# Kernel optimization log

Hardware: AMD Instinct MI355X
Metric: run time of the kernel (lower is better)

## Reference

```python
import jax, jax.numpy as jnp
import numpy as np

E = 128  # embedding dim (edim)
NEG_INF = -1e8


def setup_inputs() -> dict:
    key = jax.random.key(0)
    ks = jax.random.split(key, 12)
    n_users, n_items, B, L = 100000, 50000, 4096, 64
    s = 1.0 / np.sqrt(2 * E)
    return {
        "user_embs": jax.random.normal(ks[0], (n_users, E), jnp.float32),
        "item_embs": jax.random.normal(ks[1], (n_items, E), jnp.float32),
        "w_uu": jax.random.normal(ks[2], (2 * E,), jnp.float32) * s,
        "w_uiu": jax.random.normal(ks[3], (2 * E,), jnp.float32) * s,
        "w_uui": jax.random.normal(ks[4], (2 * E,), jnp.float32) * s,
        "W0": jax.random.normal(ks[5], (E, E // 2), jnp.float32) / np.sqrt(E),
        "b0": jax.random.normal(ks[6], (E // 2,), jnp.float32) * 0.01,
        "w1": jax.random.normal(ks[7], (E // 2,), jnp.float32) / np.sqrt(E // 2),
        "uid": jax.random.randint(ks[8], (B,), 0, n_users),
        "nbr": jax.random.randint(ks[9], (B, L), 0, n_users),
        "uiu": jax.random.randint(ks[10], (B, 2, L), 0, n_items),
        "uui": jax.random.randint(ks[11], (B, 2, L), 0, n_items),
    }


def reference(user_embs, item_embs, w_uu, w_uiu, w_uui, W0, b0, w1, uid, nbr, uiu, uui):
    self_emb = user_embs[uid][:, None, :]  # [B,1,E]

    def branch(feat, mask, w):
        # feat: [B,L,E], mask: [B,L] bool. concat([self,feat]) @ w split into two GEMVs.
        logits = self_emb @ w[:E, None] + feat @ w[E:, None]  # [B,L,1]
        logits = jax.nn.leaky_relu(logits)  # slope 0.01, matches F.leaky_relu default
        logits = logits + NEG_INF * mask[:, :, None].astype(feat.dtype)
        a = jax.nn.softmax(logits, axis=1)  # over neighbor dim
        return jax.nn.relu(jnp.sum(a * feat, axis=1))  # [B,E]

    # uu meta-path
    uu_feat = branch((self_emb + user_embs[nbr]) * 0.5, nbr == 0, w_uu)
    # uiu meta-path: row 0 = item ids, row 1 = user ids
    mp_iid, mp_uid = uiu[:, 0], uiu[:, 1]
    uiu_feat = branch((self_emb + item_embs[mp_iid] + user_embs[mp_uid]) / 3.0, mp_iid == 0, w_uiu)
    # uui meta-path: row 0 = user ids, row 1 = item ids
    mp_uid2, mp_iid2 = uui[:, 0], uui[:, 1]
    uui_feat = branch((self_emb + user_embs[mp_uid2] + item_embs[mp_iid2]) / 3.0, mp_uid2 == 0, w_uui)

    def inter(feat):
        return jnp.tanh(feat @ W0 + b0).mean(axis=0) @ w1  # scalar

    scores = jnp.stack([inter(uu_feat), inter(uiu_feat), inter(uui_feat)])
    mp = jax.nn.softmax(scores)
    return jax.nn.relu(mp[0] * uu_feat + mp[1] * uiu_feat + mp[2] * uui_feat)
```

## Files before the change

### kernel.cpp

```cpp
#include <hip/hip_runtime.h>

#define E_DIM 128
#define L_DIM 64
#define HDIM 64

__device__ __forceinline__ float waveSum(float v) {
#pragma unroll
  for (int o = 32; o > 0; o >>= 1) v += __shfl_xor(v, o);
  return v;
}
__device__ __forceinline__ float waveMax(float v) {
#pragma unroll
  for (int o = 32; o > 0; o >>= 1) v = fmaxf(v, __shfl_xor(v, o));
  return v;
}
__device__ __forceinline__ float halfSum(float v) {
#pragma unroll
  for (int o = 16; o > 0; o >>= 1) v += __shfl_xor(v, o);
  return v;
}
__device__ __forceinline__ float halfMax(float v) {
#pragma unroll
  for (int o = 16; o > 0; o >>= 1) v = fmaxf(v, __shfl_xor(v, o));
  return v;
}


__global__ __launch_bounds__(256) void convert_i8(
    const float* __restrict__ user_src, const float* __restrict__ item_src,
    signed char* __restrict__ user_q, signed char* __restrict__ item_q,
    const float* __restrict__ w_uu, const float* __restrict__ w_uiu,
    const float* __restrict__ w_uui, float2* __restrict__ qU0,
    float2* __restrict__ qU1, float2* __restrict__ qU2,
    float2* __restrict__ qI1, float2* __restrict__ qI2, int nUr, int nIr) {
  const int lane = threadIdx.x & 63;
  const int j = lane & 31;
  const int h = lane >> 5;
  const int gw = blockIdx.x * 4 + (threadIdx.x >> 6);
  const int r_all = gw * 2 + h;
  if (r_all >= nUr + nIr) return;

  const bool is_user = (r_all < nUr);
  const int r = is_user ? r_all : r_all - nUr;
  const float* src = is_user ? user_src : item_src;
  signed char* dst = is_user ? user_q : item_q;

  const float4 v = *(const float4*)(src + (long)r * E_DIM + j * 4);

  float am =
      fmaxf(fmaxf(fabsf(v.x), fabsf(v.y)), fmaxf(fabsf(v.z), fabsf(v.w)));
  am = halfMax(am);
  const float s = am * (1.0f / 127.0f);
  const float inv = (am > 0.f) ? 127.0f / am : 0.f;

  int q0 = __float2int_rn(v.x * inv);
  int q1 = __float2int_rn(v.y * inv);
  int q2 = __float2int_rn(v.z * inv);
  int q3 = __float2int_rn(v.w * inv);
  q0 = max(-127, min(127, q0));
  q1 = max(-127, min(127, q1));
  q2 = max(-127, min(127, q2));
  q3 = max(-127, min(127, q3));
  const unsigned int pk = (unsigned int)(q0 & 255) |
                          ((unsigned int)(q1 & 255) << 8) |
                          ((unsigned int)(q2 & 255) << 16) |
                          ((unsigned int)(q3 & 255) << 24);
  ((unsigned int*)dst)[(long)r * (E_DIM / 4) + j] = pk;

  const float* wA = is_user ? w_uu : w_uiu;
  const float* wB = is_user ? w_uiu : w_uui;
  const float4 a4 = *(const float4*)(wA + E_DIM + j * 4);
  const float dA = halfSum(v.x * a4.x + v.y * a4.y + v.z * a4.z + v.w * a4.w);
  const float4 b4 = *(const float4*)(wB + E_DIM + j * 4);
  const float dB = halfSum(v.x * b4.x + v.y * b4.y + v.z * b4.z + v.w * b4.w);
  float dC = 0.f;
  if (is_user) {
    const float4 c4 = *(const float4*)(w_uui + E_DIM + j * 4);
    dC = halfSum(v.x * c4.x + v.y * c4.y + v.z * c4.z + v.w * c4.w);
  }
  if (j == 0) {
    if (is_user) {
      qU0[r] = make_float2(dA, s);
      qU1[r] = make_float2(dB, s);
      qU2[r] = make_float2(dC, s);
    } else {
      qI1[r] = make_float2(dA, s);
      qI2[r] = make_float2(dB, s);
    }
  }
}

__global__ __launch_bounds__(256) void phase1_i8(
    const float* __restrict__ user_embs,
    const signed char* __restrict__ user_q,
    const signed char* __restrict__ item_q,
    const float2* __restrict__ qU0, const float2* __restrict__ qU1,
    const float2* __restrict__ qU2, const float2* __restrict__ qI1,
    const float2* __restrict__ qI2,
    const float* __restrict__ w_uu, const float* __restrict__ w_uiu,
    const float* __restrict__ w_uui, const float* __restrict__ W0,
    const float* __restrict__ b0, const float* __restrict__ w1,
    const int* __restrict__ uid, const int* __restrict__ nbr,
    const int* __restrict__ uiu, const int* __restrict__ uui,
    float* __restrict__ feats,
    float* __restrict__ partials,
    int B) {
  const int lane = threadIdx.x & 63;
  const int j = lane & 15;
  const int quarter = lane >> 4;
  const int wv = threadIdx.x >> 6;
  const int w_id = blockIdx.x * 4 + wv;
  const int b = w_id / 3;
  const int k = w_id - 3 * b;
  if (b >= B) return;

  __shared__ float sc[4][E_DIM];

  const bool is_uu = (k == 0);
  const float scale = is_uu ? 0.5f : (1.0f / 3.0f);
  const uint2* T0 = (const uint2*)((k == 1) ? item_q : user_q);
  const uint2* T1 = (const uint2*)((k == 1) ? user_q : item_q);
  const float2* P0 = (k == 0) ? qU0 : (k == 1) ? qI1 : qU2;
  const float2* P1 = (k == 1) ? qU1 : qI2;

  int i0_l, i1_l;
  if (is_uu) {
    i0_l = nbr[b * L_DIM + lane];
    i1_l = 0;
  } else {
    const int* mp = (k == 1) ? uiu : uui;
    i0_l = mp[(b * 2 + 0) * L_DIM + lane];
    i1_l = mp[(b * 2 + 1) * L_DIM + lane];
  }
  const float2 ps0 = P0[i0_l];
  float2 ps1 = make_float2(0.f, 0.f);
  if (!is_uu) ps1 = P1[i1_l];

  const int u = uid[b];
  const float2 self2 = *(const float2*)(user_embs + (long)u * E_DIM + lane * 2);

  const float* w = (k == 0) ? w_uu : (k == 1) ? w_uiu : w_uui;
  const float2 wa = *(const float2*)(w + lane * 2);
  const float2 wb = *(const float2*)(w + E_DIM + lane * 2);
  const float S1 = waveSum(self2.x * wa.x + self2.y * wa.y);
  const float S2 = waveSum(self2.x * wb.x + self2.y * wb.y);

  float d = ps0.x;
  if (!is_uu) d += ps1.x;
  float logit = S1 + scale * (S2 + d);
  logit = (logit > 0.f) ? logit : 0.01f * logit;
  if (i0_l == 0) logit += -100000000.0f;

  const float M = waveMax(logit);
  const float p = __expf(logit - M);
  const float Z = waveSum(p);
  const float a_l = p / Z;

  const float as0_l = a_l * ps0.y;
  const float as1_l = is_uu ? 0.f : a_l * ps1.y;

  constexpr int RQ = E_DIM / 8;
  float o0 = 0.f, o1 = 0.f, o2 = 0.f, o3 = 0.f;
  float o4 = 0.f, o5 = 0.f, o6 = 0.f, o7 = 0.f;

  int l4 = quarter;
  float a0c = __shfl(as0_l, l4);
  float a1c = 0.f;
  int i0 = __shfl(i0_l, l4);
  uint2 q0 = T0[(long)i0 * RQ + j];
  uint2 q1 = make_uint2(0, 0);
  if (!is_uu) {
    a1c = __shfl(as1_l, l4);
    const int i1 = __shfl(i1_l, l4);
    q1 = T1[(long)i1 * RQ + j];
  }

  for (int it = 0; it < L_DIM / 4; ++it) {
    const float a0 = a0c, a1 = a1c;
    const uint2 qa = q0, qb = q1;
    if (it < L_DIM / 4 - 1) {
      l4 = 4 * (it + 1) + quarter;
      a0c = __shfl(as0_l, l4);
      i0 = __shfl(i0_l, l4);
      q0 = T0[(long)i0 * RQ + j];
      if (!is_uu) {
        a1c = __shfl(as1_l, l4);
        const int i1 = __shfl(i1_l, l4);
        q1 = T1[(long)i1 * RQ + j];
      }
    }
    o0 += a0 * (float)(signed char)(qa.x);
    o1 += a0 * (float)(signed char)(qa.x >> 8);
    o2 += a0 * (float)(signed char)(qa.x >> 16);
    o3 += a0 * (float)((int)qa.x >> 24);
    o4 += a0 * (float)(signed char)(qa.y);
    o5 += a0 * (float)(signed char)(qa.y >> 8);
    o6 += a0 * (float)(signed char)(qa.y >> 16);
    o7 += a0 * (float)((int)qa.y >> 24);
    if (!is_uu) {
      o0 += a1 * (float)(signed char)(qb.x);
      o1 += a1 * (float)(signed char)(qb.x >> 8);
      o2 += a1 * (float)(signed char)(qb.x >> 16);
      o3 += a1 * (float)((int)qb.x >> 24);
      o4 += a1 * (float)(signed char)(qb.y);
      o5 += a1 * (float)(signed char)(qb.y >> 8);
      o6 += a1 * (float)(signed char)(qb.y >> 16);
      o7 += a1 * (float)((int)qb.y >> 24);
    }
  }
  o0 += __shfl_xor(o0, 16); o0 += __shfl_xor(o0, 32);
  o1 += __shfl_xor(o1, 16); o1 += __shfl_xor(o1, 32);
  o2 += __shfl_xor(o2, 16); o2 += __shfl_xor(o2, 32);
  o3 += __shfl_xor(o3, 16); o3 += __shfl_xor(o3, 32);
  o4 += __shfl_xor(o4, 16); o4 += __shfl_xor(o4, 32);
  o5 += __shfl_xor(o5, 16); o5 += __shfl_xor(o5, 32);
  o6 += __shfl_xor(o6, 16); o6 += __shfl_xor(o6, 32);
  o7 += __shfl_xor(o7, 16); o7 += __shfl_xor(o7, 32);

  const float4 sA = *(const float4*)(user_embs + (long)u * E_DIM + j * 8);
  const float4 sB = *(const float4*)(user_embs + (long)u * E_DIM + j * 8 + 4);
  float4 rA, rB;
  rA.x = fmaxf((sA.x + o0) * scale, 0.f);
  rA.y = fmaxf((sA.y + o1) * scale, 0.f);
  rA.z = fmaxf((sA.z + o2) * scale, 0.f);
  rA.w = fmaxf((sA.w + o3) * scale, 0.f);
  rB.x = fmaxf((sB.x + o4) * scale, 0.f);
  rB.y = fmaxf((sB.y + o5) * scale, 0.f);
  rB.z = fmaxf((sB.z + o6) * scale, 0.f);
  rB.w = fmaxf((sB.w + o7) * scale, 0.f);
  if (lane < 16) {
    float* fp = feats + ((long)k * B + b) * E_DIM + j * 8;
    *(float4*)fp = rA;
    *(float4*)(fp + 4) = rB;
    *(float4*)(&sc[wv][j * 8]) = rA;
    *(float4*)(&sc[wv][j * 8 + 4]) = rB;
  }
  __syncthreads();

  float hid = b0[lane];
#pragma unroll 4
  for (int e = 0; e < E_DIM; ++e) hid += sc[wv][e] * W0[e * HDIM + lane];
  const float pp = tanhf(hid) * w1[lane];
  const float sum = waveSum(pp);
  if (lane == 0) partials[(long)k * B + b] = sum;
}

__global__ __launch_bounds__(256) void phase1_f32(
    const float* __restrict__ user_embs, const float* __restrict__ item_embs,
    const float* __restrict__ w_uu, const float* __restrict__ w_uiu,
    const float* __restrict__ w_uui, const float* __restrict__ W0,
    const float* __restrict__ b0, const float* __restrict__ w1,
    const int* __restrict__ uid, const int* __restrict__ nbr,
    const int* __restrict__ uiu, const int* __restrict__ uui,
    float* __restrict__ feats, float* __restrict__ partials, int B) {
  const int lane = threadIdx.x & 63;
  const int wv = threadIdx.x >> 6;
  const int w_id = blockIdx.x * 4 + wv;
  const int b = w_id / 3;
  const int k = w_id - 3 * b;
  if (b >= B) return;

  __shared__ float sc[4][E_DIM];
  const int u = uid[b];
  const float self0 = user_embs[u * E_DIM + lane];
  const float self1 = user_embs[u * E_DIM + 64 + lane];
  const float* w = (k == 0) ? w_uu : (k == 1) ? w_uiu : w_uui;
  const float wa0 = w[lane], wa1 = w[64 + lane];
  const float wb0 = w[128 + lane], wb1 = w[192 + lane];
  const float logit_self = waveSum(self0 * wa0 + self1 * wa1);
  const bool is_uu = (k == 0);
  const float scale = is_uu ? 0.5f : (1.0f / 3.0f);
  const float* t0 = (k == 1) ? item_embs : user_embs;
  const float* t1 = (k == 1) ? user_embs : item_embs;
  int i0_l, i1_l;
  if (is_uu) {
    i0_l = nbr[b * L_DIM + lane];
    i1_l = 0;
  } else {
    const int* mp = (k == 1) ? uiu : uui;
    i0_l = mp[(b * 2 + 0) * L_DIM + lane];
    i1_l = mp[(b * 2 + 1) * L_DIM + lane];
  }
  const float mask_l = (i0_l == 0) ? 1.0f : 0.0f;
  float m = -3.0e38f, s = 0.0f, o0 = 0.0f, o1 = 0.0f;
  int i0 = __shfl(i0_l, 0), i1 = __shfl(i1_l, 0);
  float g00 = t0[i0 * E_DIM + lane];
  float g01 = t0[i0 * E_DIM + 64 + lane];
  float g10 = 0.f, g11 = 0.f;
  if (!is_uu) {
    g10 = t1[i1 * E_DIM + lane];
    g11 = t1[i1 * E_DIM + 64 + lane];
  }
  for (int l = 0; l < L_DIM; ++l) {
    const float f0 = (self0 + g00 + g10) * scale;
    const float f1 = (self1 + g01 + g11) * scale;
    if (l < L_DIM - 1) {
      i0 = __shfl(i0_l, l + 1);
      i1 = __shfl(i1_l, l + 1);
      g00 = t0[i0 * E_DIM + lane];
      g01 = t0[i0 * E_DIM + 64 + lane];
      if (!is_uu) {
        g10 = t1[i1 * E_DIM + lane];
        g11 = t1[i1 * E_DIM + 64 + lane];
      }
    }
    float logit = waveSum(f0 * wb0 + f1 * wb1) + logit_self;
    logit = (logit > 0.f) ? logit : 0.01f * logit;
    logit += -100000000.0f * __shfl(mask_l, l);
    const float mn = fmaxf(m, logit);
    const float alpha = __expf(m - mn);
    const float p = __expf(logit - mn);
    s = s * alpha + p;
    o0 = o0 * alpha + p * f0;
    o1 = o1 * alpha + p * f1;
    m = mn;
  }
  const float inv_s = 1.0f / s;
  const float r0 = fmaxf(o0 * inv_s, 0.f);
  const float r1 = fmaxf(o1 * inv_s, 0.f);
  feats[((long)k * B + b) * E_DIM + lane] = r0;
  feats[((long)k * B + b) * E_DIM + 64 + lane] = r1;
  sc[wv][lane] = r0;
  sc[wv][64 + lane] = r1;
  __syncthreads();
  float hid = b0[lane];
#pragma unroll 4
  for (int e = 0; e < E_DIM; ++e) hid += sc[wv][e] * W0[e * HDIM + lane];
  const float p = tanhf(hid) * w1[lane];
  const float sum = waveSum(p);
  if (lane == 0) partials[(long)k * B + b] = sum;
}

__global__ __launch_bounds__(256) void reduce_scores(
    const float* __restrict__ partials, float* __restrict__ weights, int B) {
  __shared__ float red[256];
  const int tid = threadIdx.x;
  float s[3];
#pragma unroll
  for (int k = 0; k < 3; ++k) {
    float acc = 0.f;
    for (int i = tid; i < B; i += 256) acc += partials[(long)k * B + i];
    red[tid] = acc;
    __syncthreads();
    for (int off = 128; off > 0; off >>= 1) {
      if (tid < off) red[tid] += red[tid + off];
      __syncthreads();
    }
    s[k] = red[0];
    __syncthreads();
  }
  if (tid == 0) {
    const float inv_b = 1.0f / (float)B;
    const float s0 = s[0] * inv_b, s1 = s[1] * inv_b, s2 = s[2] * inv_b;
    const float m = fmaxf(s0, fmaxf(s1, s2));
    const float e0 = __expf(s0 - m);
    const float e1 = __expf(s1 - m);
    const float e2 = __expf(s2 - m);
    const float inv = 1.0f / (e0 + e1 + e2);
    weights[0] = e0 * inv;
    weights[1] = e1 * inv;
    weights[2] = e2 * inv;
  }
}

__global__ __launch_bounds__(256) void phase2(
    const float* __restrict__ feats, const float* __restrict__ weights,
    float* __restrict__ out, int B) {
  const int i = blockIdx.x * blockDim.x + threadIdx.x;
  const int n = B * E_DIM;
  if (i >= n) return;
  const float w0 = weights[0], w1 = weights[1], w2 = weights[2];
  const float v = w0 * feats[i] + w1 * feats[n + i] + w2 * feats[2 * n + i];
  out[i] = fmaxf(v, 0.f);
}

__global__ __launch_bounds__(256) void phase2_fused(
    const float* __restrict__ partials, const float* __restrict__ feats,
    float* __restrict__ out, int B) {
  __shared__ float red[3][4];
  const int tid = threadIdx.x;
  const int lane = tid & 63;
  const int wv = tid >> 6;

  float s0 = 0.f, s1 = 0.f, s2 = 0.f;
  if ((B & 3) == 0) {
    const float4* p4 = (const float4*)partials;
    const int nb4 = B >> 2;
    for (int i = tid; i < nb4; i += 256) {
      const float4 v0 = p4[i];
      const float4 v1 = p4[nb4 + i];
      const float4 v2 = p4[2 * nb4 + i];
      s0 += (v0.x + v0.y) + (v0.z + v0.w);
      s1 += (v1.x + v1.y) + (v1.z + v1.w);
      s2 += (v2.x + v2.y) + (v2.z + v2.w);
    }
  } else {
    for (int i = tid; i < B; i += 256) {
      s0 += partials[i];
      s1 += partials[B + i];
      s2 += partials[2 * B + i];
    }
  }
  s0 = waveSum(s0);
  s1 = waveSum(s1);
  s2 = waveSum(s2);
  if (lane == 0) {
    red[0][wv] = s0;
    red[1][wv] = s1;
    red[2][wv] = s2;
  }
  __syncthreads();
  const float inv_b = 1.0f / (float)B;
  const float a0 = (red[0][0] + red[0][1] + red[0][2] + red[0][3]) * inv_b;
  const float a1 = (red[1][0] + red[1][1] + red[1][2] + red[1][3]) * inv_b;
  const float a2 = (red[2][0] + red[2][1] + red[2][2] + red[2][3]) * inv_b;
  const float m = fmaxf(a0, fmaxf(a1, a2));
  const float e0 = __expf(a0 - m);
  const float e1 = __expf(a1 - m);
  const float e2 = __expf(a2 - m);
  const float inv = 1.0f / (e0 + e1 + e2);
  const float w0 = e0 * inv, w1 = e1 * inv, w2 = e2 * inv;

  const int n4 = (B * E_DIM) >> 2;
  const float4* f4 = (const float4*)feats;
  float4* o4 = (float4*)out;
  for (int i = blockIdx.x * 256 + tid; i < n4; i += gridDim.x * 256) {
    const float4 x = f4[i];
    const float4 y = f4[n4 + i];
    const float4 z = f4[2 * n4 + i];
    float4 r;
    r.x = fmaxf(w0 * x.x + w1 * y.x + w2 * z.x, 0.f);
    r.y = fmaxf(w0 * x.y + w1 * y.y + w2 * z.y, 0.f);
    r.z = fmaxf(w0 * x.z + w1 * y.z + w2 * z.z, 0.f);
    r.w = fmaxf(w0 * x.w + w1 * y.w + w2 * z.w, 0.f);
    o4[i] = r;
  }
}

extern "C" void kernel_launch(void* const* d_in, const int* in_sizes, int n_in,
                              void* d_out, int out_size, void* d_ws,
                              size_t ws_size, hipStream_t stream) {
  const float* user_embs = (const float*)d_in[0];
  const float* item_embs = (const float*)d_in[1];
  const float* w_uu = (const float*)d_in[2];
  const float* w_uiu = (const float*)d_in[3];
  const float* w_uui = (const float*)d_in[4];
  const float* W0 = (const float*)d_in[5];
  const float* b0 = (const float*)d_in[6];
  const float* w1 = (const float*)d_in[7];
  const int* uid = (const int*)d_in[8];
  const int* nbr = (const int*)d_in[9];
  const int* uiu = (const int*)d_in[10];
  const int* uui = (const int*)d_in[11];
  const int B = in_sizes[8];
  const int nU = in_sizes[0];
  const int nI = in_sizes[1];
  const int nUr = nU / E_DIM;
  const int nIr = nI / E_DIM;

  float* ws = (float*)d_ws;
  float* partials = ws;
  float* weights = ws + 3 * B;
  float* feats = ws + 3 * B + 64;
  const size_t f32_floats = (size_t)3 * B + 64 + (size_t)3 * B * E_DIM;
  signed char* user_q = (signed char*)(ws + f32_floats);
  signed char* item_q = user_q + nU;
  size_t qwords = ((size_t)nU + nI + 3) / 4;
  qwords += (qwords & 1);
  float2* qU0 = (float2*)(ws + f32_floats + qwords);
  float2* qU1 = qU0 + nUr;
  float2* qU2 = qU1 + nUr;
  float2* qI1 = qU2 + nUr;
  float2* qI2 = qI1 + nIr;
  const size_t need =
      (f32_floats + qwords + 2 * ((size_t)3 * nUr + 2 * nIr)) * 4;

  const int n_waves = 3 * B;
  const int n_blocks = (n_waves + 3) / 4;
  const int n = B * E_DIM;

  if (ws_size >= need) {
    const int conv_waves = (nUr + nIr + 1) / 2;
    convert_i8<<<(conv_waves + 3) / 4, 256, 0, stream>>>(
        user_embs, item_embs, user_q, item_q, w_uu, w_uiu, w_uui, qU0, qU1,
        qU2, qI1, qI2, nUr, nIr);
    phase1_i8<<<n_blocks, 256, 0, stream>>>(
        user_embs, user_q, item_q, qU0, qU1, qU2, qI1, qI2, w_uu, w_uiu,
        w_uui, W0, b0, w1, uid, nbr, uiu, uui, feats, partials, B);
    phase2_fused<<<256, 256, 0, stream>>>(partials, feats, (float*)d_out, B);
  } else {
    phase1_f32<<<n_blocks, 256, 0, stream>>>(user_embs, item_embs, w_uu,
                                             w_uiu, w_uui, W0, b0, w1, uid,
                                             nbr, uiu, uui, feats, partials, B);
    reduce_scores<<<1, 256, 0, stream>>>(partials, weights, B);
    phase2<<<(n + 255) / 256, 256, 0, stream>>>(feats, weights, (float*)d_out,
                                                B);
  }
}
```

Baseline: 185.0 us.

## Deepen gather prefetch to four stages and group uu waves separately

The gather loop over neighbors now keeps four row loads in flight instead of one, through a fully unrolled rotating register pipeline. This is meant to hide the latency of the random int8 embedding gathers. The wave-to-(batch, branch) mapping also changes: all uu waves come first, followed by interleaved uiu/uui pairs. Within a block, the cheaper uu waves are then no longer mixed with the two-table branches, which should reduce divergence in per-block work. Holding more loads in flight raises register pressure and may lower occupancy.

```diff
diff --git a/kernel.cpp b/kernel.cpp
--- a/kernel.cpp
+++ b/kernel.cpp
@@ -110,9 +110,17 @@
   const int quarter = lane >> 4;
   const int wv = threadIdx.x >> 6;
   const int w_id = blockIdx.x * 4 + wv;
-  const int b = w_id / 3;
-  const int k = w_id - 3 * b;
-  if (b >= B) return;
+  if (w_id >= 3 * B) return;
+
+  int b, k;
+  if (w_id < B) {
+    b = w_id;
+    k = 0;
+  } else {
+    const int t = w_id - B;
+    b = t >> 1;
+    k = 1 + (t & 1);
+  }
 
   __shared__ float sc[4][E_DIM];
 
@@ -163,32 +171,21 @@
   float o0 = 0.f, o1 = 0.f, o2 = 0.f, o3 = 0.f;
   float o4 = 0.f, o5 = 0.f, o6 = 0.f, o7 = 0.f;
 
-  int l4 = quarter;
-  float a0c = __shfl(as0_l, l4);
-  float a1c = 0.f;
-  int i0 = __shfl(i0_l, l4);
-  uint2 q0 = T0[(long)i0 * RQ + j];
-  uint2 q1 = make_uint2(0, 0);
-  if (!is_uu) {
-    a1c = __shfl(as1_l, l4);
-    const int i1 = __shfl(i1_l, l4);
-    q1 = T1[(long)i1 * RQ + j];
-  }
-
-  for (int it = 0; it < L_DIM / 4; ++it) {
-    const float a0 = a0c, a1 = a1c;
-    const uint2 qa = q0, qb = q1;
-    if (it < L_DIM / 4 - 1) {
-      l4 = 4 * (it + 1) + quarter;
-      a0c = __shfl(as0_l, l4);
-      i0 = __shfl(i0_l, l4);
-      q0 = T0[(long)i0 * RQ + j];
-      if (!is_uu) {
-        a1c = __shfl(as1_l, l4);
-        const int i1 = __shfl(i1_l, l4);
-        q1 = T1[(long)i1 * RQ + j];
-      }
-    }
+  auto LD = [&](int g, float& w0o, float& w1o, uint2& r0o, uint2& r1o) {
+    const int l4 = 4 * g + quarter;
+    w0o = __shfl(as0_l, l4);
+    const int i0g = __shfl(i0_l, l4);
+    r0o = T0[(long)i0g * RQ + j];
+    if (!is_uu) {
+      w1o = __shfl(as1_l, l4);
+      const int i1g = __shfl(i1_l, l4);
+      r1o = T1[(long)i1g * RQ + j];
+    } else {
+      w1o = 0.f;
+      r1o = make_uint2(0u, 0u);
+    }
+  };
+  auto FMA8 = [&](float a0, float a1, uint2 qa, uint2 qb) {
     o0 += a0 * (float)(signed char)(qa.x);
     o1 += a0 * (float)(signed char)(qa.x >> 8);
     o2 += a0 * (float)(signed char)(qa.x >> 16);
@@ -206,6 +203,40 @@
       o5 += a1 * (float)(signed char)(qb.y >> 8);
       o6 += a1 * (float)(signed char)(qb.y >> 16);
       o7 += a1 * (float)((int)qb.y >> 24);
+    }
+  };
+
+  float aA0, aA1, aB0, aB1, aC0, aC1, aD0, aD1;
+  uint2 qA0, qA1, qB0, qB1, qC0, qC1, qD0, qD1;
+  LD(0, aA0, aA1, qA0, qA1);
+  LD(1, aB0, aB1, qB0, qB1);
+  LD(2, aC0, aC1, qC0, qC1);
+  LD(3, aD0, aD1, qD0, qD1);
+#pragma unroll
+  for (int it = 0; it < L_DIM / 4; it += 4) {
+    {
+      const float a0 = aA0, a1 = aA1;
+      const uint2 qa = qA0, qb = qA1;
+      if (it + 4 < L_DIM / 4) LD(it + 4, aA0, aA1, qA0, qA1);
+      FMA8(a0, a1, qa, qb);
+    }
+    {
+      const float a0 = aB0, a1 = aB1;
+      const uint2 qa = qB0, qb = qB1;
+      if (it + 5 < L_DIM / 4) LD(it + 5, aB0, aB1, qB0, qB1);
+      FMA8(a0, a1, qa, qb);
+    }
+    {
+      const float a0 = aC0, a1 = aC1;
+      const uint2 qa = qC0, qb = qC1;
+      if (it + 6 < L_DIM / 4) LD(it + 6, aC0, aC1, qC0, qC1);
+      FMA8(a0, a1, qa, qb);
+    }
+    {
+      const float a0 = aD0, a1 = aD1;
+      const uint2 qa = qD0, qb = qD1;
+      if (it + 7 < L_DIM / 4) LD(it + 7, aD0, aD1, qD0, qD1);
+      FMA8(a0, a1, qa, qb);
     }
   }
   o0 += __shfl_xor(o0, 16); o0 += __shfl_xor(o0, 32);
```

Result: faster. 180.7 us (-2.3%).
